# Kernel tuning notes

Hardware: AMD Instinct MI355X
Metric: run time of the kernel (lower is better)

The kernel has to match this reference:

```python
import jax, jax.numpy as jnp
import numpy as np

N, C = 2, 256
GH0, GW0 = 40, 40
GH1, GW1 = 40, 40
STRIDE, TOPK = 2, 8
TEMP, THRESH, BORDER = 0.1, 0.2, 2
H0, W0 = GH0 * STRIDE, GW0 * STRIDE
H1, W1 = GH1 * STRIDE, GW1 * STRIDE
K4 = TOPK * STRIDE * STRIDE
# create_meshgrid(2,2) flattened: entries (x, y) in row-major (y outer) order
GRID = jnp.array([[0, 0], [1, 0], [0, 1], [1, 1]], dtype=jnp.int32)


def map_indices(idx, size0, size1):
    # idx: (n, G0, topk) coarse indices into image1 coarse grid
    row = idx[..., None] // size1[1] * STRIDE + GRID[:, 1]
    col = idx[..., None] % size1[1] * STRIDE + GRID[:, 0]
    fine = row * (size1[1] * STRIDE) + col  # (n, G0, topk, 4)
    n = idx.shape[0]
    fine = fine.reshape(n, size0[0], 1, size0[1], 1, -1)
    fine = jnp.broadcast_to(fine, (n, size0[0], STRIDE, size0[1], STRIDE, fine.shape[-1]))
    return fine.reshape(n, size0[0] * size0[1] * STRIDE * STRIDE, -1)


def remove_border_one_side(idx, br, size):
    h, w = size
    pos = jnp.arange(h * w)
    r, c = pos // w, pos % w
    border = (r < br) | (r >= h - br) | (c < br) | (c >= w - br)
    return jnp.where(border[None, :], 0, idx)


def unpatchify(x, grid, stride):
    n, g, s2, c = x.shape
    gh, gw = grid
    x = x.reshape(n, gh, gw, stride, stride, c)
    x = jnp.transpose(x, (0, 5, 1, 3, 2, 4))
    return x.reshape(n, c, gh * stride, gw * stride)


def fused_heatmaps(x0, x1, a01, a10, ind0_f, ind1_f):
    s01 = jnp.einsum('ngqc,ngkc->ngqk', x0, a01) / C  # (n, G0, 4, K4)
    s10 = jnp.einsum('ngqc,ngkc->ngqk', x1, a10) / C
    h01 = jax.nn.softmax(s01 / TEMP, axis=-1)
    h10 = jax.nn.softmax(s10 / TEMP, axis=-1)
    h01 = h01.reshape(N, GH0, GW0, STRIDE, STRIDE, K4)
    h01 = jnp.transpose(h01, (0, 1, 3, 2, 4, 5)).reshape(N, H0 * W0, K4)
    h10 = h10.reshape(N, GH1, GW1, STRIDE, STRIDE, K4)
    h10 = jnp.transpose(h10, (0, 5, 1, 3, 2, 4)).reshape(N, K4, H1 * W1)
    # dense scatter + gather mutual fusion (as in the torch code)
    b = jnp.arange(N)[:, None, None]
    l1 = jnp.arange(H1 * W1)[None, None, :]
    Z0 = jnp.zeros((N, H0 * W0, H1 * W1), h10.dtype).at[b, ind1_f, l1].set(h10)
    new_h01 = h01 * jnp.take_along_axis(Z0, ind0_f, axis=-1)
    l0 = jnp.arange(H0 * W0)[None, :, None]
    Z1 = jnp.zeros((N, H0 * W0, H1 * W1), h01.dtype).at[b, l0, ind0_f].set(h01)
    new_h10 = h10 * jnp.take_along_axis(Z1, ind1_f, axis=-2)
    return new_h01, new_h10


def coarse_matching(h01, h10, ind0_f, ind1_f):
    score = jnp.max(h01, axis=-1)                 # (n, L0)
    sub0 = jnp.argmax(h01, axis=-1)               # (n, L0)
    j_best = jnp.take_along_axis(ind0_f, sub0[..., None], axis=-1)[..., 0]
    sub1 = jnp.argmax(h10, axis=-2)               # (n, L1)
    i_best = jnp.take_along_axis(ind1_f, sub1[:, None, :], axis=-2)[:, 0, :]
    j_best = remove_border_one_side(j_best, BORDER, (H1, W1))
    i_best = remove_border_one_side(i_best, BORDER, (H0, W0))
    biproj = jnp.take_along_axis(i_best, j_best, axis=-1)
    mask = biproj == jnp.arange(H0 * W0)[None, :]
    mask = mask.at[:, 0].set(False)
    mask = mask & (score > THRESH)
    scores = jnp.where(mask, score, 0.0)
    return mask, j_best, scores


def setup_inputs() -> dict:
    key = jax.random.key(0)
    ks = jax.random.split(key, 6)
    return {
        'x0': jax.random.normal(ks[0], (N, GH0 * GW0, 4, C), jnp.float32),
        'x1': jax.random.normal(ks[1], (N, GH1 * GW1, 4, C), jnp.float32),
        'attended0_to_1': jax.random.normal(ks[2], (N, GH0 * GW0, K4, C), jnp.float32),
        'attended1_to_0': jax.random.normal(ks[3], (N, GH1 * GW1, K4, C), jnp.float32),
        'x0_prior': jax.random.normal(ks[4], (N, C, GH0, GW0), jnp.float32),
        'x1_prior': jax.random.normal(ks[5], (N, C, GH1, GW1), jnp.float32),
    }


def reference(x0, x1, attended0_to_1, attended1_to_0, x0_prior, x1_prior):
    p0 = x0_prior.reshape(N, C, GH0 * GW0)
    p1 = x1_prior.reshape(N, C, GH1 * GW1)
    sim = jnp.einsum('nci,ncj->nij', p0, p1) / C  # (n, G0, G1)
    _, i01 = jax.lax.top_k(sim, TOPK)                              # (n, G0, topk)
    _, i10 = jax.lax.top_k(jnp.swapaxes(sim, -2, -1), TOPK)        # (n, G1, topk)
    ind0_f = map_indices(i01, (GH0, GW0), (GH1, GW1))              # (n, L0, K4)
    ind1_f = jnp.swapaxes(map_indices(i10, (GH1, GW1), (GH0, GW0)), -2, -1)  # (n, K4, L1)
    h01, h10 = fused_heatmaps(x0, x1, attended0_to_1, attended1_to_0, ind0_f, ind1_f)
    mask, j_best, scores = coarse_matching(jax.lax.stop_gradient(h01), jax.lax.stop_gradient(h10), ind0_f, ind1_f)
    x0_8x = unpatchify(x0, (GH0, GW0), STRIDE)
    x1_8x = unpatchify(x1, (GH1, GW1), STRIDE)
    return h01, h10, scores, j_best, mask, x0_8x, x1_8x
```

## Files before the change

### kernel.cpp

```cpp
#include <hip/hip_runtime.h>


#define N_B   2
#define C_DIM 256
#define G0N   1600
#define GW    40
#define L0N   6400
#define W_F   80
#define TK    8

__global__ __launch_bounds__(256) void k_sim(const float* __restrict__ p0,
                                             const float* __restrict__ p1,
                                             float* __restrict__ sim,
                                             float* __restrict__ simT) {
  const int n  = blockIdx.z;
  const int i0 = blockIdx.y * 128;
  const int j0 = blockIdx.x * 128;
  const float* A = p0 + (size_t)n * C_DIM * G0N;
  const float* B = p1 + (size_t)n * C_DIM * G0N;
  __shared__ float As[16][128];
  __shared__ float Bs[16][128];
  const int t  = threadIdx.x;
  const int tx = t & 15, ty = t >> 4;
  const int lf = t & 31;
  const int lr = t >> 5;

  float acc[8][8];
#pragma unroll
  for (int a = 0; a < 8; ++a)
#pragma unroll
    for (int b = 0; b < 8; ++b) acc[a][b] = 0.f;

  int ia = i0 + lf * 4; if (ia > G0N - 4) ia = G0N - 4;
  int ja = j0 + lf * 4; if (ja > G0N - 4) ja = G0N - 4;

  for (int kc = 0; kc < C_DIM; kc += 16) {
#pragma unroll
    for (int p = 0; p < 2; ++p) {
      int row = lr + p * 8;
      int c = kc + row;
      float4 av = *(const float4*)(A + (size_t)c * G0N + ia);
      float4 bv = *(const float4*)(B + (size_t)c * G0N + ja);
      *(float4*)&As[row][lf * 4] = av;
      *(float4*)&Bs[row][lf * 4] = bv;
    }
    __syncthreads();
#pragma unroll
    for (int k = 0; k < 16; ++k) {
      float a[8], b[8];
      *(float4*)&a[0] = *(const float4*)&As[k][ty * 8];
      *(float4*)&a[4] = *(const float4*)&As[k][ty * 8 + 4];
      *(float4*)&b[0] = *(const float4*)&Bs[k][tx * 8];
      *(float4*)&b[4] = *(const float4*)&Bs[k][tx * 8 + 4];
#pragma unroll
      for (int ii = 0; ii < 8; ++ii)
#pragma unroll
        for (int jj = 0; jj < 8; ++jj) acc[ii][jj] += a[ii] * b[jj];
    }
    __syncthreads();
  }

  float* simn  = sim  + (size_t)n * G0N * G0N;
  float* simTn = simT + (size_t)n * G0N * G0N;
#pragma unroll
  for (int ii = 0; ii < 8; ++ii) {
    int i = i0 + ty * 8 + ii;
    if (i < G0N) {
#pragma unroll
      for (int j4 = 0; j4 < 2; ++j4) {
        int j = j0 + tx * 8 + j4 * 4;
        if (j < G0N) {
          float4 v = make_float4(acc[ii][j4*4], acc[ii][j4*4+1], acc[ii][j4*4+2], acc[ii][j4*4+3]);
          *(float4*)(simn + (size_t)i * G0N + j) = v;
        }
      }
    }
  }
#pragma unroll
  for (int jj = 0; jj < 8; ++jj) {
    int j = j0 + tx * 8 + jj;
    if (j < G0N) {
#pragma unroll
      for (int i4 = 0; i4 < 2; ++i4) {
        int i = i0 + ty * 8 + i4 * 4;
        if (i < G0N) {
          float4 v = make_float4(acc[i4*4][jj], acc[i4*4+1][jj], acc[i4*4+2][jj], acc[i4*4+3][jj]);
          *(float4*)(simTn + (size_t)j * G0N + i) = v;
        }
      }
    }
  }
}

__global__ __launch_bounds__(256) void k_topk(const float* __restrict__ sim,
                                              const float* __restrict__ simT,
                                              int* __restrict__ i01,
                                              int* __restrict__ i10) {
  int wid  = (blockIdx.x * 256 + threadIdx.x) >> 6;
  int lane = threadIdx.x & 63;
  int dir  = wid / (N_B * G0N);
  int r    = wid - dir * (N_B * G0N);
  const float* row = (dir ? simT : sim) + (size_t)r * G0N;
  int* out = (dir ? i10 : i01) + r * TK;

  float v[25];
#pragma unroll
  for (int tt = 0; tt < 25; ++tt) v[tt] = row[lane + 64 * tt];

#pragma unroll 1
  for (int k = 0; k < TK; ++k) {
    float best = -3.4e38f; int bidx = 0x7fffffff;
#pragma unroll
    for (int tt = 0; tt < 25; ++tt) {
      if (v[tt] > best) { best = v[tt]; bidx = lane + 64 * tt; }
    }
#pragma unroll
    for (int off = 1; off < 64; off <<= 1) {
      float ov = __shfl_xor(best, off);
      int   oi = __shfl_xor(bidx, off);
      if (ov > best || (ov == best && oi < bidx)) { best = ov; bidx = oi; }
    }
    if (lane == 0) out[k] = bidx;
#pragma unroll
    for (int tt = 0; tt < 25; ++tt)
      if (lane + 64 * tt == bidx) v[tt] = -3.4e38f;
  }
}

__global__ __launch_bounds__(128) void k_heat(const float* __restrict__ x,
                                              const float* __restrict__ att,
                                              float* __restrict__ hpre) {
  const int ng = blockIdx.x;
  const float* xp = x   + (size_t)ng * 4  * C_DIM;
  const float* ap = att + (size_t)ng * 32 * C_DIM;
  __shared__ float xs[4 * C_DIM];
  __shared__ float as[32][260];
  const int t = threadIdx.x;
#pragma unroll
  for (int j = 0; j < 16; ++j) {
    int f = t + j * 128;
    float4 v = *(const float4*)(ap + (size_t)f * 4);
    *(float4*)&as[f >> 6][(f & 63) * 4] = v;
  }
#pragma unroll
  for (int j = 0; j < 2; ++j) {
    int f = t + j * 128;
    *(float4*)&xs[f * 4] = *(const float4*)(xp + (size_t)f * 4);
  }
  __syncthreads();
  const int k4 = t & 31, q = t >> 5;
  float acc = 0.f;
#pragma unroll
  for (int c4 = 0; c4 < 64; ++c4) {
    float4 a  = *(const float4*)&as[k4][c4 * 4];
    float4 xv = *(const float4*)&xs[q * C_DIM + c4 * 4];
    acc += a.x * xv.x + a.y * xv.y + a.z * xv.z + a.w * xv.w;
  }
  float l = (acc * (1.0f / 256.0f)) / 0.1f;
  float m = l;
#pragma unroll
  for (int off = 1; off < 32; off <<= 1) m = fmaxf(m, __shfl_xor(m, off));
  float e = expf(l - m);
  float s = e;
#pragma unroll
  for (int off = 1; off < 32; off <<= 1) s += __shfl_xor(s, off);
  hpre[(size_t)ng * 128 + q * 32 + k4] = e / s;
}

__global__ __launch_bounds__(256) void k_fuse01(const float* __restrict__ h01p,
                                                const float* __restrict__ h10p,
                                                const int* __restrict__ i01,
                                                const int* __restrict__ i10,
                                                float* __restrict__ h01_out,
                                                float* __restrict__ score_ws,
                                                int* __restrict__ jbest_ws,
                                                float* __restrict__ jbest_out) {
  int idx = blockIdx.x * 8 + (threadIdx.x >> 5);
  int k4  = threadIdx.x & 31;
  int n = idx / L0N, l0 = idx - n * L0N;
  int r0 = l0 / W_F, c0 = l0 - r0 * W_F;
  int g0 = (r0 >> 1) * GW + (c0 >> 1);
  int q0 = ((r0 & 1) << 1) | (c0 & 1);
  int k = k4 >> 2, g = k4 & 3;
  int jc = i01[(n * G0N + g0) * TK + k];
  const int* row10 = i10 + (n * G0N + jc) * TK;
  int kf = -1;
#pragma unroll
  for (int kp = 0; kp < 8; ++kp) if (row10[kp] == g0) kf = kp;
  float m = 0.f;
  if (kf >= 0) m = h10p[((n * G0N + jc) * 4 + g) * 32 + kf * 4 + q0];
  float h = h01p[((n * G0N + g0) * 4 + q0) * 32 + k4];
  float val = h * m;
  h01_out[(size_t)idx * 32 + k4] = val;

  float best = val; int bi = k4;
#pragma unroll
  for (int off = 1; off < 32; off <<= 1) {
    float ov = __shfl_xor(best, off);
    int   oi = __shfl_xor(bi, off);
    if (ov > best || (ov == best && oi < bi)) { best = ov; bi = oi; }
  }
  if (k4 == 0) {
    score_ws[idx] = best;
    int kB = bi >> 2, gB = bi & 3;
    int jcB = i01[(n * G0N + g0) * TK + kB];
    int jrow = jcB / GW;
    int jb = ((jrow * 2 + (gB >> 1)) * W_F) + (jcB - jrow * GW) * 2 + (gB & 1);
    if (r0 < 2 || r0 >= W_F - 2 || c0 < 2 || c0 >= W_F - 2) jb = 0;
    jbest_ws[idx]  = jb;
    jbest_out[idx] = (float)jb;
  }
}

__global__ __launch_bounds__(256) void k_fuse10(const float* __restrict__ h01p,
                                                const float* __restrict__ h10p,
                                                const int* __restrict__ i01,
                                                const int* __restrict__ i10,
                                                float* __restrict__ h10_out,
                                                int* __restrict__ ibest_ws) {
  int idx = blockIdx.x * 8 + (threadIdx.x >> 5);
  int k4  = threadIdx.x & 31;
  int n = idx / L0N, l1 = idx - n * L0N;
  int r1 = l1 / W_F, c1 = l1 - r1 * W_F;
  int g1 = (r1 >> 1) * GW + (c1 >> 1);
  int q1 = ((r1 & 1) << 1) | (c1 & 1);
  int k = k4 >> 2, g = k4 & 3;
  int ic = i10[(n * G0N + g1) * TK + k];
  const int* row01 = i01 + (n * G0N + ic) * TK;
  int kf = -1;
#pragma unroll
  for (int kp = 0; kp < 8; ++kp) if (row01[kp] == g1) kf = kp;
  float m = 0.f;
  if (kf >= 0) m = h01p[((n * G0N + ic) * 4 + g) * 32 + kf * 4 + q1];
  float h = h10p[((n * G0N + g1) * 4 + q1) * 32 + k4];
  float val = h * m;
  h10_out[((size_t)n * 32 + k4) * L0N + l1] = val;

  float best = val; int bi = k4;
#pragma unroll
  for (int off = 1; off < 32; off <<= 1) {
    float ov = __shfl_xor(best, off);
    int   oi = __shfl_xor(bi, off);
    if (ov > best || (ov == best && oi < bi)) { best = ov; bi = oi; }
  }
  if (k4 == 0) {
    int kB = bi >> 2, gB = bi & 3;
    int icB = i10[(n * G0N + g1) * TK + kB];
    int irow = icB / GW;
    int ib = ((irow * 2 + (gB >> 1)) * W_F) + (icB - irow * GW) * 2 + (gB & 1);
    if (r1 < 2 || r1 >= W_F - 2 || c1 < 2 || c1 >= W_F - 2) ib = 0;
    ibest_ws[idx] = ib;
  }
}

__global__ __launch_bounds__(256) void k_final(const float* __restrict__ score_ws,
                                               const int* __restrict__ jbest_ws,
                                               const int* __restrict__ ibest_ws,
                                               float* __restrict__ scores_out,
                                               float* __restrict__ mask_out) {
  int idx = blockIdx.x * 256 + threadIdx.x;
  if (idx >= N_B * L0N) return;
  int n = idx / L0N, l0 = idx - n * L0N;
  int jb = jbest_ws[idx];
  float sc = score_ws[idx];
  int biproj = ibest_ws[n * L0N + jb];
  bool mk = (biproj == l0) && (l0 != 0) && (sc > 0.2f);
  scores_out[idx] = mk ? sc : 0.f;
  mask_out[idx]   = mk ? 1.f : 0.f;
}

__global__ __launch_bounds__(256) void k_unpatch(const float* __restrict__ x,
                                                 float* __restrict__ out) {
  __shared__ float tile[32][33];
  int cc0 = blockIdx.x * 32;
  int r   = blockIdx.y;
  int n   = blockIdx.z >> 3;
  int c0  = (blockIdx.z & 7) * 32;
  int t = threadIdx.x;
  int sr = r & 1, ghr = r >> 1;
  int pos = t >> 5, cl = t & 31;
#pragma unroll
  for (int it = 0; it < 4; ++it) {
    int p = pos + it * 8;
    int cc = cc0 + p;
    if (cc < W_F) {
      int gg = ghr * GW + (cc >> 1);
      int qq = (sr << 1) | (cc & 1);
      tile[p][cl] = x[(((size_t)n * G0N + gg) * 4 + qq) * C_DIM + c0 + cl];
    }
  }
  __syncthreads();
  int co = t >> 5, p2 = t & 31;
#pragma unroll
  for (int it = 0; it < 4; ++it) {
    int c = c0 + co + it * 8;
    int cc = cc0 + p2;
    if (cc < W_F)
      out[(((size_t)n * C_DIM + c) * W_F + r) * W_F + cc] = tile[p2][co + it * 8];
  }
}

extern "C" void kernel_launch(void* const* d_in, const int* in_sizes, int n_in,
                              void* d_out, int out_size, void* d_ws, size_t ws_size,
                              hipStream_t stream) {
  const float* x0  = (const float*)d_in[0];
  const float* x1  = (const float*)d_in[1];
  const float* a01 = (const float*)d_in[2];
  const float* a10 = (const float*)d_in[3];
  const float* p0  = (const float*)d_in[4];
  const float* p1  = (const float*)d_in[5];
  float* out = (float*)d_out;

  float* ws       = (float*)d_ws;
  float* sim      = ws;
  float* simT     = ws + 5120000;
  int*   i01      = (int*)(ws + 10240000);
  int*   i10      = (int*)(ws + 10265600);
  float* h01p     = ws + 10291200;
  float* h10p     = ws + 10700800;
  float* score_ws = ws + 11110400;
  int*   jbest_ws = (int*)(ws + 11123200);
  int*   ibest_ws = (int*)(ws + 11136000);

  float* o_h01   = out;
  float* o_h10   = out + 409600;
  float* o_score = out + 819200;
  float* o_jbest = out + 832000;
  float* o_mask  = out + 844800;
  float* o_x08   = out + 857600;
  float* o_x18   = out + 4134400;

  k_sim<<<dim3(13, 13, 2), 256, 0, stream>>>(p0, p1, sim, simT);
  k_topk<<<1600, 256, 0, stream>>>(sim, simT, i01, i10);
  k_heat<<<3200, 128, 0, stream>>>(x0, a01, h01p);
  k_heat<<<3200, 128, 0, stream>>>(x1, a10, h10p);
  k_fuse01<<<1600, 256, 0, stream>>>(h01p, h10p, i01, i10, o_h01, score_ws, jbest_ws, o_jbest);
  k_fuse10<<<1600, 256, 0, stream>>>(h01p, h10p, i01, i10, o_h10, ibest_ws);
  k_final<<<50, 256, 0, stream>>>(score_ws, jbest_ws, ibest_ws, o_score, o_mask);
  k_unpatch<<<dim3(3, 80, 16), 256, 0, stream>>>(x0, o_x08);
  k_unpatch<<<dim3(3, 80, 16), 256, 0, stream>>>(x1, o_x18);
}
```

Baseline: 360.6 us.

## Rewrite similarity GEMM as per-wave tiles and merge paired kernel launches

Replaces the shared-memory tiled similarity GEMM with a per-wave kernel in which each wave computes a 32x64 tile. Each lane holds 32 accumulators and reads A rows as uniform broadcast loads, and the kernel now applies the 1/C scale. It also merges the two heatmap launches, the two fuse launches and the two unpatchify launches into single launches that pick their direction from the block index. The heatmap kernel now splits the channel dot product across two half-waves and combines them with a shuffle. The aim is to cut launch count and improve GEMM occupancy, at the risk of losing shared-memory data reuse in the GEMM.

```diff
diff --git a/kernel.cpp b/kernel.cpp
--- a/kernel.cpp
+++ b/kernel.cpp
@@ -9,87 +9,45 @@
 #define W_F   80
 #define TK    8
 
-__global__ __launch_bounds__(256) void k_sim(const float* __restrict__ p0,
-                                             const float* __restrict__ p1,
-                                             float* __restrict__ sim,
-                                             float* __restrict__ simT) {
-  const int n  = blockIdx.z;
-  const int i0 = blockIdx.y * 128;
-  const int j0 = blockIdx.x * 128;
-  const float* A = p0 + (size_t)n * C_DIM * G0N;
-  const float* B = p1 + (size_t)n * C_DIM * G0N;
-  __shared__ float As[16][128];
-  __shared__ float Bs[16][128];
-  const int t  = threadIdx.x;
-  const int tx = t & 15, ty = t >> 4;
-  const int lf = t & 31;
-  const int lr = t >> 5;
-
-  float acc[8][8];
-#pragma unroll
-  for (int a = 0; a < 8; ++a)
-#pragma unroll
-    for (int b = 0; b < 8; ++b) acc[a][b] = 0.f;
-
-  int ia = i0 + lf * 4; if (ia > G0N - 4) ia = G0N - 4;
-  int ja = j0 + lf * 4; if (ja > G0N - 4) ja = G0N - 4;
-
-  for (int kc = 0; kc < C_DIM; kc += 16) {
-#pragma unroll
-    for (int p = 0; p < 2; ++p) {
-      int row = lr + p * 8;
-      int c = kc + row;
-      float4 av = *(const float4*)(A + (size_t)c * G0N + ia);
-      float4 bv = *(const float4*)(B + (size_t)c * G0N + ja);
-      *(float4*)&As[row][lf * 4] = av;
-      *(float4*)&Bs[row][lf * 4] = bv;
-    }
-    __syncthreads();
-#pragma unroll
-    for (int k = 0; k < 16; ++k) {
-      float a[8], b[8];
-      *(float4*)&a[0] = *(const float4*)&As[k][ty * 8];
-      *(float4*)&a[4] = *(const float4*)&As[k][ty * 8 + 4];
-      *(float4*)&b[0] = *(const float4*)&Bs[k][tx * 8];
-      *(float4*)&b[4] = *(const float4*)&Bs[k][tx * 8 + 4];
-#pragma unroll
-      for (int ii = 0; ii < 8; ++ii)
-#pragma unroll
-        for (int jj = 0; jj < 8; ++jj) acc[ii][jj] += a[ii] * b[jj];
-    }
-    __syncthreads();
-  }
+__global__ __launch_bounds__(256) void k_sim2(const float* __restrict__ p0,
+                                              const float* __restrict__ p1,
+                                              float* __restrict__ sim,
+                                              float* __restrict__ simT) {
+  const int w    = threadIdx.x >> 6;
+  const int lane = threadIdx.x & 63;
+  const int tile = blockIdx.x * 4 + w;
+  const int n    = tile / 1250;
+  const int rem  = tile - n * 1250;
+  const int it   = rem / 25, jt = rem - it * 25;
+  const int i0   = it * 32, j0 = jt * 64;
+
+  const float* A = p0 + (size_t)n * C_DIM * G0N + i0;
+  const float* B = p1 + (size_t)n * C_DIM * G0N + j0 + lane;
+
+  float acc[32];
+#pragma unroll
+  for (int r = 0; r < 32; ++r) acc[r] = 0.f;
+
+#pragma unroll 2
+  for (int k = 0; k < C_DIM; ++k) {
+    const float bv = B[(size_t)k * G0N];
+    const float* Ak = A + (size_t)k * G0N;
+#pragma unroll
+    for (int r = 0; r < 32; ++r) acc[r] = fmaf(Ak[r], bv, acc[r]);
+  }
+
+#pragma unroll
+  for (int r = 0; r < 32; ++r) acc[r] *= (1.0f / 256.0f);
 
   float* simn  = sim  + (size_t)n * G0N * G0N;
   float* simTn = simT + (size_t)n * G0N * G0N;
 #pragma unroll
-  for (int ii = 0; ii < 8; ++ii) {
-    int i = i0 + ty * 8 + ii;
-    if (i < G0N) {
-#pragma unroll
-      for (int j4 = 0; j4 < 2; ++j4) {
-        int j = j0 + tx * 8 + j4 * 4;
-        if (j < G0N) {
-          float4 v = make_float4(acc[ii][j4*4], acc[ii][j4*4+1], acc[ii][j4*4+2], acc[ii][j4*4+3]);
-          *(float4*)(simn + (size_t)i * G0N + j) = v;
-        }
-      }
-    }
-  }
-#pragma unroll
-  for (int jj = 0; jj < 8; ++jj) {
-    int j = j0 + tx * 8 + jj;
-    if (j < G0N) {
-#pragma unroll
-      for (int i4 = 0; i4 < 2; ++i4) {
-        int i = i0 + ty * 8 + i4 * 4;
-        if (i < G0N) {
-          float4 v = make_float4(acc[i4*4][jj], acc[i4*4+1][jj], acc[i4*4+2][jj], acc[i4*4+3][jj]);
-          *(float4*)(simTn + (size_t)j * G0N + i) = v;
-        }
-      }
-    }
-  }
+  for (int r = 0; r < 32; ++r)
+    simn[(size_t)(i0 + r) * G0N + j0 + lane] = acc[r];
+  float* trow = simTn + (size_t)(j0 + lane) * G0N + i0;
+  const float4* av = (const float4*)acc;
+#pragma unroll
+  for (int c = 0; c < 8; ++c) *(float4*)(trow + c * 4) = av[c];
 }
 
 __global__ __launch_bounds__(256) void k_topk(const float* __restrict__ sim,
@@ -127,35 +85,50 @@
   }
 }
 
-__global__ __launch_bounds__(128) void k_heat(const float* __restrict__ x,
-                                              const float* __restrict__ att,
-                                              float* __restrict__ hpre) {
-  const int ng = blockIdx.x;
+__global__ __launch_bounds__(256) void k_heat2(const float* __restrict__ x0,
+                                               const float* __restrict__ a01,
+                                               const float* __restrict__ x1,
+                                               const float* __restrict__ a10,
+                                               float* __restrict__ h01p,
+                                               float* __restrict__ h10p) {
+  const int bid = blockIdx.x;
+  const int d   = bid / 3200;
+  const int ng  = bid - d * 3200;
+  const float* x   = d ? x1  : x0;
+  const float* att = d ? a10 : a01;
+  float*       hp  = d ? h10p : h01p;
   const float* xp = x   + (size_t)ng * 4  * C_DIM;
   const float* ap = att + (size_t)ng * 32 * C_DIM;
+
+  __shared__ float as[32][260];
   __shared__ float xs[4 * C_DIM];
-  __shared__ float as[32][260];
   const int t = threadIdx.x;
 #pragma unroll
-  for (int j = 0; j < 16; ++j) {
-    int f = t + j * 128;
+  for (int j = 0; j < 8; ++j) {
+    int f = t + j * 256;
     float4 v = *(const float4*)(ap + (size_t)f * 4);
     *(float4*)&as[f >> 6][(f & 63) * 4] = v;
   }
-#pragma unroll
-  for (int j = 0; j < 2; ++j) {
-    int f = t + j * 128;
-    *(float4*)&xs[f * 4] = *(const float4*)(xp + (size_t)f * 4);
+  {
+    float4 v = *(const float4*)(xp + (size_t)t * 4);
+    *(float4*)&xs[t * 4] = v;
   }
   __syncthreads();
-  const int k4 = t & 31, q = t >> 5;
+
+  const int q = t >> 6;
+  const int lane = t & 63;
+  const int k4 = lane & 31, ch = lane >> 5;
+  const float* ar = &as[k4][ch * 128];
+  const float* xr = &xs[q * C_DIM + ch * 128];
   float acc = 0.f;
 #pragma unroll
-  for (int c4 = 0; c4 < 64; ++c4) {
-    float4 a  = *(const float4*)&as[k4][c4 * 4];
-    float4 xv = *(const float4*)&xs[q * C_DIM + c4 * 4];
+  for (int c4 = 0; c4 < 32; ++c4) {
+    float4 a  = *(const float4*)(ar + c4 * 4);
+    float4 xv = *(const float4*)(xr + c4 * 4);
     acc += a.x * xv.x + a.y * xv.y + a.z * xv.z + a.w * xv.w;
   }
+  acc += __shfl_xor(acc, 32);
+
   float l = (acc * (1.0f / 256.0f)) / 0.1f;
   float m = l;
 #pragma unroll
@@ -164,92 +137,85 @@
   float s = e;
 #pragma unroll
   for (int off = 1; off < 32; off <<= 1) s += __shfl_xor(s, off);
-  hpre[(size_t)ng * 128 + q * 32 + k4] = e / s;
-}
-
-__global__ __launch_bounds__(256) void k_fuse01(const float* __restrict__ h01p,
-                                                const float* __restrict__ h10p,
-                                                const int* __restrict__ i01,
-                                                const int* __restrict__ i10,
-                                                float* __restrict__ h01_out,
-                                                float* __restrict__ score_ws,
-                                                int* __restrict__ jbest_ws,
-                                                float* __restrict__ jbest_out) {
-  int idx = blockIdx.x * 8 + (threadIdx.x >> 5);
+  if (ch == 0) hp[(size_t)ng * 128 + q * 32 + k4] = e / s;
+}
+
+__global__ __launch_bounds__(256) void k_fuse(const float* __restrict__ h01p,
+                                              const float* __restrict__ h10p,
+                                              const int* __restrict__ i01,
+                                              const int* __restrict__ i10,
+                                              float* __restrict__ h01_out,
+                                              float* __restrict__ h10_out,
+                                              float* __restrict__ score_ws,
+                                              int* __restrict__ jbest_ws,
+                                              float* __restrict__ jbest_out,
+                                              int* __restrict__ ibest_ws) {
+  const int d   = blockIdx.x / 1600;
+  const int sub = blockIdx.x - d * 1600;
+  int idx = sub * 8 + (threadIdx.x >> 5);
   int k4  = threadIdx.x & 31;
-  int n = idx / L0N, l0 = idx - n * L0N;
-  int r0 = l0 / W_F, c0 = l0 - r0 * W_F;
-  int g0 = (r0 >> 1) * GW + (c0 >> 1);
-  int q0 = ((r0 & 1) << 1) | (c0 & 1);
-  int k = k4 >> 2, g = k4 & 3;
-  int jc = i01[(n * G0N + g0) * TK + k];
-  const int* row10 = i10 + (n * G0N + jc) * TK;
-  int kf = -1;
-#pragma unroll
-  for (int kp = 0; kp < 8; ++kp) if (row10[kp] == g0) kf = kp;
-  float m = 0.f;
-  if (kf >= 0) m = h10p[((n * G0N + jc) * 4 + g) * 32 + kf * 4 + q0];
-  float h = h01p[((n * G0N + g0) * 4 + q0) * 32 + k4];
-  float val = h * m;
-  h01_out[(size_t)idx * 32 + k4] = val;
-
-  float best = val; int bi = k4;
-#pragma unroll
-  for (int off = 1; off < 32; off <<= 1) {
-    float ov = __shfl_xor(best, off);
-    int   oi = __shfl_xor(bi, off);
-    if (ov > best || (ov == best && oi < bi)) { best = ov; bi = oi; }
-  }
-  if (k4 == 0) {
-    score_ws[idx] = best;
-    int kB = bi >> 2, gB = bi & 3;
-    int jcB = i01[(n * G0N + g0) * TK + kB];
-    int jrow = jcB / GW;
-    int jb = ((jrow * 2 + (gB >> 1)) * W_F) + (jcB - jrow * GW) * 2 + (gB & 1);
-    if (r0 < 2 || r0 >= W_F - 2 || c0 < 2 || c0 >= W_F - 2) jb = 0;
-    jbest_ws[idx]  = jb;
-    jbest_out[idx] = (float)jb;
-  }
-}
-
-__global__ __launch_bounds__(256) void k_fuse10(const float* __restrict__ h01p,
-                                                const float* __restrict__ h10p,
-                                                const int* __restrict__ i01,
-                                                const int* __restrict__ i10,
-                                                float* __restrict__ h10_out,
-                                                int* __restrict__ ibest_ws) {
-  int idx = blockIdx.x * 8 + (threadIdx.x >> 5);
-  int k4  = threadIdx.x & 31;
-  int n = idx / L0N, l1 = idx - n * L0N;
-  int r1 = l1 / W_F, c1 = l1 - r1 * W_F;
-  int g1 = (r1 >> 1) * GW + (c1 >> 1);
-  int q1 = ((r1 & 1) << 1) | (c1 & 1);
-  int k = k4 >> 2, g = k4 & 3;
-  int ic = i10[(n * G0N + g1) * TK + k];
-  const int* row01 = i01 + (n * G0N + ic) * TK;
-  int kf = -1;
-#pragma unroll
-  for (int kp = 0; kp < 8; ++kp) if (row01[kp] == g1) kf = kp;
-  float m = 0.f;
-  if (kf >= 0) m = h01p[((n * G0N + ic) * 4 + g) * 32 + kf * 4 + q1];
-  float h = h10p[((n * G0N + g1) * 4 + q1) * 32 + k4];
-  float val = h * m;
-  h10_out[((size_t)n * 32 + k4) * L0N + l1] = val;
-
-  float best = val; int bi = k4;
-#pragma unroll
-  for (int off = 1; off < 32; off <<= 1) {
-    float ov = __shfl_xor(best, off);
-    int   oi = __shfl_xor(bi, off);
-    if (ov > best || (ov == best && oi < bi)) { best = ov; bi = oi; }
-  }
-  if (k4 == 0) {
-    int kB = bi >> 2, gB = bi & 3;
-    int icB = i10[(n * G0N + g1) * TK + kB];
-    int irow = icB / GW;
-    int ib = ((irow * 2 + (gB >> 1)) * W_F) + (icB - irow * GW) * 2 + (gB & 1);
-    if (r1 < 2 || r1 >= W_F - 2 || c1 < 2 || c1 >= W_F - 2) ib = 0;
-    ibest_ws[idx] = ib;
+  int n = idx / L0N, l = idx - n * L0N;
+  int rr = l / W_F, cc = l - rr * W_F;
+  int g = (rr >> 1) * GW + (cc >> 1);
+  int q = ((rr & 1) << 1) | (cc & 1);
+  int k = k4 >> 2, gg = k4 & 3;
+
+  if (d == 0) {
+    int jc = i01[(n * G0N + g) * TK + k];
+    const int* row10 = i10 + (n * G0N + jc) * TK;
+    int kf = -1;
+#pragma unroll
+    for (int kp = 0; kp < 8; ++kp) if (row10[kp] == g) kf = kp;
+    float m = 0.f;
+    if (kf >= 0) m = h10p[((n * G0N + jc) * 4 + gg) * 32 + kf * 4 + q];
+    float h = h01p[((n * G0N + g) * 4 + q) * 32 + k4];
+    float val = h * m;
+    h01_out[(size_t)idx * 32 + k4] = val;
+
+    float best = val; int bi = k4;
+#pragma unroll
+    for (int off = 1; off < 32; off <<= 1) {
+      float ov = __shfl_xor(best, off);
+      int   oi = __shfl_xor(bi, off);
+      if (ov > best || (ov == best && oi < bi)) { best = ov; bi = oi; }
+    }
+    if (k4 == 0) {
+      score_ws[idx] = best;
+      int kB = bi >> 2, gB = bi & 3;
+      int jcB = i01[(n * G0N + g) * TK + kB];
+      int jrow = jcB / GW;
+      int jb = ((jrow * 2 + (gB >> 1)) * W_F) + (jcB - jrow * GW) * 2 + (gB & 1);
+      if (rr < 2 || rr >= W_F - 2 || cc < 2 || cc >= W_F - 2) jb = 0;
+      jbest_ws[idx]  = jb;
+      jbest_out[idx] = (float)jb;
+    }
+  } else {
+    int ic = i10[(n * G0N + g) * TK + k];
+    const int* row01 = i01 + (n * G0N + ic) * TK;
+    int kf = -1;
+#pragma unroll
+    for (int kp = 0; kp < 8; ++kp) if (row01[kp] == g) kf = kp;
+    float m = 0.f;
+    if (kf >= 0) m = h01p[((n * G0N + ic) * 4 + gg) * 32 + kf * 4 + q];
+    float h = h10p[((n * G0N + g) * 4 + q) * 32 + k4];
+    float val = h * m;
+    h10_out[((size_t)n * 32 + k4) * L0N + l] = val;
+
+    float best = val; int bi = k4;
+#pragma unroll
+    for (int off = 1; off < 32; off <<= 1) {
+      float ov = __shfl_xor(best, off);
+      int   oi = __shfl_xor(bi, off);
+      if (ov > best || (ov == best && oi < bi)) { best = ov; bi = oi; }
+    }
+    if (k4 == 0) {
+      int kB = bi >> 2, gB = bi & 3;
+      int icB = i10[(n * G0N + g) * TK + kB];
+      int irow = icB / GW;
+      int ib = ((irow * 2 + (gB >> 1)) * W_F) + (icB - irow * GW) * 2 + (gB & 1);
+      if (rr < 2 || rr >= W_F - 2 || cc < 2 || cc >= W_F - 2) ib = 0;
+      ibest_ws[idx] = ib;
+    }
   }
 }
 
@@ -269,13 +235,19 @@
   mask_out[idx]   = mk ? 1.f : 0.f;
 }
 
-__global__ __launch_bounds__(256) void k_unpatch(const float* __restrict__ x,
-                                                 float* __restrict__ out) {
+__global__ __launch_bounds__(256) void k_unpatch2(const float* __restrict__ x0,
+                                                  const float* __restrict__ x1,
+                                                  float* __restrict__ o0,
+                                                  float* __restrict__ o1) {
   __shared__ float tile[32][33];
+  int which = blockIdx.z >> 4;
+  const float* x = which ? x1 : x0;
+  float* out = which ? o1 : o0;
+  int zz  = blockIdx.z & 15;
   int cc0 = blockIdx.x * 32;
   int r   = blockIdx.y;
-  int n   = blockIdx.z >> 3;
-  int c0  = (blockIdx.z & 7) * 32;
+  int n   = zz >> 3;
+  int c0  = (zz & 7) * 32;
   int t = threadIdx.x;
   int sr = r & 1, ghr = r >> 1;
   int pos = t >> 5, cl = t & 31;
@@ -330,13 +302,11 @@
   float* o_x08   = out + 857600;
   float* o_x18   = out + 4134400;
 
-  k_sim<<<dim3(13, 13, 2), 256, 0, stream>>>(p0, p1, sim, simT);
+  k_sim2<<<625, 256, 0, stream>>>(p0, p1, sim, simT);
   k_topk<<<1600, 256, 0, stream>>>(sim, simT, i01, i10);
-  k_heat<<<3200, 128, 0, stream>>>(x0, a01, h01p);
-  k_heat<<<3200, 128, 0, stream>>>(x1, a10, h10p);
-  k_fuse01<<<1600, 256, 0, stream>>>(h01p, h10p, i01, i10, o_h01, score_ws, jbest_ws, o_jbest);
-  k_fuse10<<<1600, 256, 0, stream>>>(h01p, h10p, i01, i10, o_h10, ibest_ws);
+  k_heat2<<<6400, 256, 0, stream>>>(x0, a01, x1, a10, h01p, h10p);
+  k_fuse<<<3200, 256, 0, stream>>>(h01p, h10p, i01, i10,
+                                   o_h01, o_h10, score_ws, jbest_ws, o_jbest, ibest_ws);
   k_final<<<50, 256, 0, stream>>>(score_ws, jbest_ws, ibest_ws, o_score, o_mask);
-  k_unpatch<<<dim3(3, 80, 16), 256, 0, stream>>>(x0, o_x08);
-  k_unpatch<<<dim3(3, 80, 16), 256, 0, stream>>>(x1, o_x18);
-}
+  k_unpatch2<<<dim3(3, 80, 32), 256, 0, stream>>>(x0, x1, o_x08, o_x18);
+}
```

After: 547.6 us. +51.9%, slower.
